# Kernel optimization log

Hardware: AMD Instinct MI355X
Metric: run time of the kernel (lower is better)

## Reference

```python
import jax, jax.numpy as jnp
import numpy as np

N = 30000      # nodes
E = 480000     # edges (no self loops; GATConv adds them)
IN = 256       # in_features
OUT = 128      # out_features == per-head channels (concat=False)
H = 4          # heads
NEG_SLOPE = 0.2


def setup_inputs() -> dict:
    key = jax.random.key(0)
    k = jax.random.split(key, 6)
    x = jax.random.normal(k[0], (N, IN), dtype=jnp.float32)
    src = jax.random.randint(k[1], (E,), 0, N, dtype=jnp.int32)
    # guarantee no self loops (GATConv would strip them before re-adding)
    off = jax.random.randint(k[2], (E,), 1, N, dtype=jnp.int32)
    dst = (src + off) % N
    edge_index = jnp.stack([src, dst])  # [2, E]
    W = jax.random.normal(k[3], (IN, H * OUT), dtype=jnp.float32) / np.float32(np.sqrt(IN))
    att_src = jax.random.normal(k[4], (H, OUT), dtype=jnp.float32) / np.float32(np.sqrt(OUT))
    att_dst = jax.random.normal(k[5], (H, OUT), dtype=jnp.float32) / np.float32(np.sqrt(OUT))
    bias = jnp.zeros((OUT,), dtype=jnp.float32)
    return {"x": x, "edge_index": edge_index, "W": W,
            "att_src": att_src, "att_dst": att_dst, "bias": bias}


def reference(x, edge_index, W, att_src, att_dst, bias):
    n = x.shape[0]
    # dense projection -> per-head features [N, H, C]
    h = (x @ W).reshape(n, H, OUT)
    a_s = jnp.einsum('nhc,hc->nh', h, att_src)  # [N, H]
    a_d = jnp.einsum('nhc,hc->nh', h, att_dst)  # [N, H]
    # add self loops (GATConv default add_self_loops=True)
    loop = jnp.arange(n, dtype=edge_index.dtype)
    src = jnp.concatenate([edge_index[0], loop])  # [Et]
    dst = jnp.concatenate([edge_index[1], loop])  # [Et]
    # per-edge attention logits + LeakyReLU
    alpha = jax.nn.leaky_relu(a_s[src] + a_d[dst], NEG_SLOPE)  # [Et, H]
    # segment softmax over incoming edges of each dst node
    amax = jax.ops.segment_max(alpha, dst, num_segments=n)      # [N, H]
    ex = jnp.exp(alpha - amax[dst])
    denom = jax.ops.segment_sum(ex, dst, num_segments=n)        # [N, H]
    w = ex / denom[dst]                                          # [Et, H]
    # gather source features, weight, scatter-add to dst
    msg = h[src] * w[:, :, None]                                 # [Et, H, C]
    out = jax.ops.segment_sum(msg, dst, num_segments=n)          # [N, H, C]
    # concat=False -> mean over heads, then bias, then module's tanh
    out = out.mean(axis=1) + bias                                # [N, C]
    return jnp.tanh(out)
```

## Files before the change

kernel.cpp:

```cpp
#include <hip/hip_runtime.h>
#include <math.h>

#define IN_F   256
#define OUT_F  128
#define HEADS  4
#define HD     (HEADS * OUT_F)
#define K2     1024
#define NEG    0.2f
#define CAP    64

typedef __attribute__((ext_vector_type(8))) short short8;
typedef __attribute__((ext_vector_type(4))) float f32x4;
typedef __attribute__((ext_vector_type(2))) float f32x2;

typedef __attribute__((address_space(1))) const void* gp_t;
typedef __attribute__((address_space(3))) void* lp_t;

static __device__ __forceinline__ ushort f2bf(float f) {
    union { float f; unsigned u; } v; v.f = f;
    unsigned r = (v.u + 0x7FFFu + ((v.u >> 16) & 1u)) >> 16;
    return (ushort)r;
}
static __device__ __forceinline__ float bflo(unsigned u) {
    union { unsigned u; float f; } v; v.u = u << 16; return v.f;
}
static __device__ __forceinline__ float bfhi(unsigned u) {
    union { unsigned u; float f; } v; v.u = u & 0xFFFF0000u; return v.f;
}

#define PKFMA(D, A, B) asm("v_pk_fma_f32 %0, %1, %2, %0" : "+v"(D) : "v"(A), "v"(B))

__global__ __launch_bounds__(256) void prep1(const float* __restrict__ W,
                                             const float* __restrict__ att_src,
                                             const float* __restrict__ att_dst,
                                             ushort* __restrict__ WT2,
                                             float* __restrict__ va_s,
                                             float* __restrict__ va_d,
                                             int* __restrict__ cursor,
                                             int n_nodes) {
    const int b = blockIdx.x;
    const int tid = threadIdx.x;
    if (b < 512) {
        int idx = b * 256 + tid;
        int cout = idx >> 10, kk = idx & 1023;
        int h = kk >> 8, c = kk & 255;
        WT2[idx] = f2bf(W[(size_t)c * HD + h * OUT_F + cout]);
    } else if (b < 768) {
        const int lane = tid & 63;
        const int p = (b - 512) * 4 + (tid >> 6);
        const int h = p >> 8;
        const int k = p & 255;
        const float* wr = W + (size_t)k * HD + h * OUT_F;
        float w0 = wr[lane], w1 = wr[lane + 64];
        float s0 = att_src[h * OUT_F + lane], s1 = att_src[h * OUT_F + lane + 64];
        float d0 = att_dst[h * OUT_F + lane], d1 = att_dst[h * OUT_F + lane + 64];
        float ss = w0 * s0 + w1 * s1;
        float sd = w0 * d0 + w1 * d1;
#pragma unroll
        for (int off = 32; off > 0; off >>= 1) {
            ss += __shfl_xor(ss, off, 64);
            sd += __shfl_xor(sd, off, 64);
        }
        if (lane == 0) { va_s[p] = ss; va_d[p] = sd; }
    } else {
        int i = (b - 768) * 256 + tid;
        if (i < n_nodes) cursor[i] = 0;
    }
}

__global__ __launch_bounds__(256) void prep2(const float* __restrict__ X,
                                             const float* __restrict__ va_s,
                                             const float* __restrict__ va_d,
                                             const int* __restrict__ src,
                                             const int* __restrict__ dst,
                                             ushort* __restrict__ Xb,
                                             float* __restrict__ a_s,
                                             float* __restrict__ a_d,
                                             int* __restrict__ cursor,
                                             int* __restrict__ table,
                                             int n_nodes, int n_edges, int nebk) {
    const int b = blockIdx.x;
    const int tid = threadIdx.x;
    if (b < nebk) {
        int e = b * 256 + tid;
        if (e < n_edges) {
            int d = dst[e];
            int r = atomicAdd(&cursor[d], 1);
            if (r < CAP) table[(size_t)d * CAP + r] = src[e];
        }
        return;
    }
    const int lane = tid & 63;
    const int node = (b - nebk) * 4 + (tid >> 6);
    if (node >= n_nodes) return;
    float4 v = *(const float4*)(X + (size_t)node * IN_F + lane * 4);
    ushort4 o; o.x = f2bf(v.x); o.y = f2bf(v.y); o.z = f2bf(v.z); o.w = f2bf(v.w);
    *(ushort4*)(Xb + (size_t)node * IN_F + lane * 4) = o;

    float ps[HEADS], pd[HEADS];
#pragma unroll
    for (int hd = 0; hd < HEADS; ++hd) {
        float4 s4 = *(const float4*)(va_s + hd * IN_F + lane * 4);
        float4 d4 = *(const float4*)(va_d + hd * IN_F + lane * 4);
        ps[hd] = v.x * s4.x + v.y * s4.y + v.z * s4.z + v.w * s4.w;
        pd[hd] = v.x * d4.x + v.y * d4.y + v.z * d4.z + v.w * d4.w;
    }
#pragma unroll
    for (int off = 32; off > 0; off >>= 1) {
#pragma unroll
        for (int hd = 0; hd < HEADS; ++hd) {
            ps[hd] += __shfl_xor(ps[hd], off, 64);
            pd[hd] += __shfl_xor(pd[hd], off, 64);
        }
    }
    if (lane == 0) {
        float4 s4 = make_float4(ps[0], ps[1], ps[2], ps[3]);
        float4 d4 = make_float4(pd[0], pd[1], pd[2], pd[3]);
        *(float4*)(a_s + node * 4) = s4;
        *(float4*)(a_d + node * 4) = d4;
    }
}

#define EDGE(E8)                                                            \
    {                                                                       \
        uint2 uu = *(const uint2*)(cons + (E8) * 512);                      \
        float4 wA = *(const float4*)(wp + (E8) * 8);                        \
        float4 wB = *(const float4*)(wp + (E8) * 8 + 4);                    \
        f32x2 f01 = {bflo(uu.x), bfhi(uu.x)};                               \
        f32x2 f23 = {bflo(uu.y), bfhi(uu.y)};                               \
        f32x2 w0p = {wA.x, wA.y}, w1p = {wA.z, wA.w};                       \
        f32x2 w2p = {wB.x, wB.y}, w3p = {wB.z, wB.w};                       \
        PKFMA(a01[0], f01, w0p); PKFMA(a23[0], f23, w0p);                   \
        PKFMA(a01[1], f01, w1p); PKFMA(a23[1], f23, w1p);                   \
        PKFMA(a01[2], f01, w2p); PKFMA(a23[2], f23, w2p);                   \
        PKFMA(a01[3], f01, w3p); PKFMA(a23[3], f23, w3p);                   \
    }

#define ISSUE(EB, DST)                                                      \
    {                                                                       \
        asm volatile("s_waitcnt lgkmcnt(0)" ::: "memory");                  \
        int s0_ = __shfl(sreg, (EB) + 0, 64);                               \
        int s1_ = __shfl(sreg, (EB) + 1, 64);                               \
        int s2_ = __shfl(sreg, (EB) + 2, 64);                               \
        int s3_ = __shfl(sreg, (EB) + 3, 64);                               \
        int s4_ = __shfl(sreg, (EB) + 4, 64);                               \
        int s5_ = __shfl(sreg, (EB) + 5, 64);                               \
        int s6_ = __shfl(sreg, (EB) + 6, 64);                               \
        int s7_ = __shfl(sreg, (EB) + 7, 64);                               \
        int sa_ = (lane & 32) ? s1_ : s0_;                                  \
        int sb_ = (lane & 32) ? s3_ : s2_;                                  \
        int sc_ = (lane & 32) ? s5_ : s4_;                                  \
        int sd_ = (lane & 32) ? s7_ : s6_;                                  \
        __builtin_amdgcn_global_load_lds((gp_t)(xb16 + (size_t)sa_ * 256),  \
                                         (lp_t)((DST) + 0 * 1024), 16, 0, 0);\
        __builtin_amdgcn_global_load_lds((gp_t)(xb16 + (size_t)sb_ * 256),  \
                                         (lp_t)((DST) + 1 * 1024), 16, 0, 0);\
        __builtin_amdgcn_global_load_lds((gp_t)(xb16 + (size_t)sc_ * 256),  \
                                         (lp_t)((DST) + 2 * 1024), 16, 0, 0);\
        __builtin_amdgcn_global_load_lds((gp_t)(xb16 + (size_t)sd_ * 256),  \
                                         (lp_t)((DST) + 3 * 1024), 16, 0, 0);\
    }

__global__ __launch_bounds__(256) void gat_agg(const ushort* __restrict__ Xb,
                                               const float* __restrict__ a_s,
                                               const float* __restrict__ a_d,
                                               const int* __restrict__ cursor,
                                               const int* __restrict__ table,
                                               ushort* __restrict__ Zb,
                                               int n_nodes) {
    __shared__ ushort xst[4][2][8][256];
    __shared__ float wse[4][CAP][8];
    const int lane = threadIdx.x & 63;
    const int wid  = threadIdx.x >> 6;
    const int n = blockIdx.x * 4 + wid;
    if (n >= n_nodes) return;
    int deg = cursor[n]; if (deg > CAP) deg = CAP;
    const int* row = table + (size_t)n * CAP;
    const bool act = lane < deg;
    int sreg = act ? row[lane] : n;

    const ushort* xb16 = Xb + (lane & 31) * 8;
    const uint2* xb2 = (const uint2*)Xb;
    uint2 uself = xb2[(size_t)n * 64 + lane];

    char* xb0 = (char*)&xst[wid][0][0][0];
    char* xb1 = (char*)&xst[wid][1][0][0];

    const int ntiles = (deg + 7) >> 3;
    if (ntiles > 0) ISSUE(0, xb0);

    const float4 ad4 = *(const float4*)(a_d + n * 4);
    const float4 as4 = *(const float4*)(a_s + n * 4);
    const float ad[4] = {ad4.x, ad4.y, ad4.z, ad4.w};
    float aself[4];
    {
        const float asn[4] = {as4.x, as4.y, as4.z, as4.w};
#pragma unroll
        for (int hd = 0; hd < 4; ++hd) {
            float al0 = asn[hd] + ad[hd];
            aself[hd] = al0 > 0.f ? al0 : NEG * al0;
        }
    }
    float al[4];
    {
        float4 av = *(const float4*)(a_s + (size_t)sreg * 4);
        const float as_[4] = {av.x, av.y, av.z, av.w};
#pragma unroll
        for (int hd = 0; hd < 4; ++hd) {
            float a = as_[hd] + ad[hd];
            a = a > 0.f ? a : NEG * a;
            al[hd] = act ? a : -1e30f;
        }
    }
    float m[4];
#pragma unroll
    for (int hd = 0; hd < 4; ++hd) m[hd] = al[hd];
#pragma unroll
    for (int off = 32; off > 0; off >>= 1)
#pragma unroll
        for (int hd = 0; hd < 4; ++hd)
            m[hd] = fmaxf(m[hd], __shfl_xor(m[hd], off, 64));
#pragma unroll
    for (int hd = 0; hd < 4; ++hd) m[hd] = fmaxf(m[hd], aself[hd]);

    float w[4], den[4];
#pragma unroll
    for (int hd = 0; hd < 4; ++hd) {
        w[hd] = act ? __expf(al[hd] - m[hd]) : 0.f;
        den[hd] = w[hd];
    }
#pragma unroll
    for (int off = 32; off > 0; off >>= 1)
#pragma unroll
        for (int hd = 0; hd < 4; ++hd)
            den[hd] += __shfl_xor(den[hd], off, 64);

    float es[4], rdv[4];
#pragma unroll
    for (int hd = 0; hd < 4; ++hd) {
        es[hd] = __expf(aself[hd] - m[hd]);
        rdv[hd] = 1.f / (den[hd] + es[hd]);
    }

    *(float4*)&wse[wid][lane][0] = make_float4(w[0], w[0], w[1], w[1]);
    *(float4*)&wse[wid][lane][4] = make_float4(w[2], w[2], w[3], w[3]);

    f32x2 a01[4], a23[4];
    {
        f32x2 s01 = {bflo(uself.x), bfhi(uself.x)};
        f32x2 s23 = {bflo(uself.y), bfhi(uself.y)};
#pragma unroll
        for (int hd = 0; hd < 4; ++hd) {
            f32x2 eh = {es[hd], es[hd]};
            a01[hd] = s01 * eh;
            a23[hd] = s23 * eh;
        }
    }
#pragma unroll 1
    for (int t = 0; t < ntiles; ++t) {
        if (t + 1 < ntiles) {
            ISSUE((t + 1) * 8, ((t + 1) & 1) ? xb1 : xb0);
            asm volatile("s_waitcnt vmcnt(4)" ::: "memory");
        } else {
            asm volatile("s_waitcnt vmcnt(0)" ::: "memory");
        }
        const char* cons = ((t & 1) ? xb1 : xb0) + lane * 8;
        const float* wp = &wse[wid][t * 8][0];
        EDGE(0); EDGE(1); EDGE(2); EDGE(3);
        EDGE(4); EDGE(5); EDGE(6); EDGE(7);
    }

    ushort* zr = Zb + (size_t)n * K2;
#pragma unroll
    for (int hd = 0; hd < 4; ++hd) {
        f32x2 r2 = {rdv[hd], rdv[hd]};
        f32x2 z01 = a01[hd] * r2;
        f32x2 z23 = a23[hd] * r2;
        ushort4 z;
        z.x = f2bf(z01.x); z.y = f2bf(z01.y);
        z.z = f2bf(z23.x); z.w = f2bf(z23.y);
        *(ushort4*)(zr + hd * 256 + lane * 4) = z;
    }
}

#define GBM 32
#define GBN 128
#define GBK 64

__global__ __launch_bounds__(256) void gemm2(const ushort* __restrict__ Zb,
                                             const ushort* __restrict__ WT2,
                                             const float* __restrict__ bias,
                                             float* __restrict__ out,
                                             int n_nodes) {
    __shared__ ushort As[2][GBM][GBK];
    __shared__ ushort Bs[2][GBN][GBK];
    const int tid = threadIdx.x;
    const int m0 = blockIdx.y * GBM;
    const int wave = tid >> 6, lane = tid & 63;
    const int wm = (wave & 1) * 16, wn = (wave >> 1) * 64;
    const int l15 = lane & 15, quad = lane >> 4;

    const int rr8 = lane >> 3;
    const int cg  = (lane & 7) ^ rr8;
    const ushort* gA0 = Zb + (size_t)(m0 + wave * 8 + rr8) * K2 + cg * 8;
    const ushort* gB0 = WT2 + (size_t)(wave * 32 + rr8) * K2 + cg * 8;
    const ushort* gB1 = gB0 + 8 * K2;
    const ushort* gB2 = gB0 + 16 * K2;
    const ushort* gB3 = gB0 + 24 * K2;

#define STAGE(T, B)                                                          \
    {                                                                        \
        const int ko_ = (T) * GBK;                                           \
        __builtin_amdgcn_global_load_lds((gp_t)(gA0 + ko_),                  \
            (lp_t)&As[B][wave * 8][0], 16, 0, 0);                            \
        __builtin_amdgcn_global_load_lds((gp_t)(gB0 + ko_),                  \
            (lp_t)&Bs[B][wave * 32][0], 16, 0, 0);                           \
        __builtin_amdgcn_global_load_lds((gp_t)(gB1 + ko_),                  \
            (lp_t)&Bs[B][wave * 32 + 8][0], 16, 0, 0);                       \
        __builtin_amdgcn_global_load_lds((gp_t)(gB2 + ko_),                  \
            (lp_t)&Bs[B][wave * 32 + 16][0], 16, 0, 0);                      \
        __builtin_amdgcn_global_load_lds((gp_t)(gB3 + ko_),                  \
            (lp_t)&Bs[B][wave * 32 + 24][0], 16, 0, 0);                      \
    }

    f32x4 acc[4];
#pragma unroll
    for (int j = 0; j < 4; ++j) acc[j] = (f32x4){0.f, 0.f, 0.f, 0.f};

    const int NT = K2 / GBK;
    STAGE(0, 0);
#pragma unroll 1
    for (int t = 0; t < NT; ++t) {
        const int b = t & 1;
        if (t + 1 < NT) {
            STAGE(t + 1, b ^ 1);
            asm volatile("s_waitcnt vmcnt(5)" ::: "memory");
        } else {
            asm volatile("s_waitcnt vmcnt(0)" ::: "memory");
        }
        asm volatile("s_barrier" ::: "memory");

#pragma unroll
        for (int tt = 0; tt < 2; ++tt) {
            const int sl = ((tt * 4 + quad) ^ (l15 & 7)) * 8;
            short8 af = *(const short8*)&As[b][wm + l15][sl];
            short8 bf_[4];
#pragma unroll
            for (int fn = 0; fn < 4; ++fn)
                bf_[fn] = *(const short8*)&Bs[b][wn + fn * 16 + l15][sl];
#pragma unroll
            for (int fn = 0; fn < 4; ++fn)
                acc[fn] = __builtin_amdgcn_mfma_f32_16x16x32_bf16(
                    af, bf_[fn], acc[fn], 0, 0, 0);
        }
        asm volatile("s_barrier" ::: "memory");
    }

    float bcol[4];
#pragma unroll
    for (int fn = 0; fn < 4; ++fn) bcol[fn] = bias[wn + fn * 16 + l15];

    int gmb = m0 + wm + quad * 4;
#pragma unroll
    for (int reg = 0; reg < 4; ++reg) {
        int gm = gmb + reg;
        if (gm < n_nodes) {
#pragma unroll
            for (int fn = 0; fn < 4; ++fn) {
                float o = tanhf(0.25f * acc[fn][reg] + bcol[fn]);
                out[(size_t)gm * OUT_F + wn + fn * 16 + l15] = o;
            }
        }
    }
}

extern "C" void kernel_launch(void* const* d_in, const int* in_sizes, int n_in,
                              void* d_out, int out_size, void* d_ws, size_t ws_size,
                              hipStream_t stream) {
    const float* x       = (const float*)d_in[0];
    const int*   ei      = (const int*)d_in[1];
    const float* W       = (const float*)d_in[2];
    const float* att_src = (const float*)d_in[3];
    const float* att_dst = (const float*)d_in[4];
    const float* bias    = (const float*)d_in[5];
    float* out = (float*)d_out;

    const int n_nodes = in_sizes[0] / IN_F;
    const int n_edges = in_sizes[1] / 2;
    const int* src = ei;
    const int* dst = ei + n_edges;

    char* ws = (char*)d_ws;
    size_t off = 0;
    auto alloc = [&](size_t bytes) -> void* {
        void* p = ws + off;
        off = (off + bytes + 255) & ~(size_t)255;
        return p;
    };
    ushort* Xb     = (ushort*)alloc((size_t)n_nodes * IN_F * sizeof(ushort));
    ushort* Zb     = (ushort*)alloc((size_t)n_nodes * K2 * sizeof(ushort));
    ushort* WT2    = (ushort*)alloc((size_t)OUT_F * K2 * sizeof(ushort));
    float*  va_s   = (float*)alloc((size_t)HEADS * IN_F * sizeof(float));
    float*  va_d   = (float*)alloc((size_t)HEADS * IN_F * sizeof(float));
    float*  a_s    = (float*)alloc((size_t)n_nodes * HEADS * sizeof(float));
    float*  a_d    = (float*)alloc((size_t)n_nodes * HEADS * sizeof(float));
    int*    cursor = (int*)alloc((size_t)n_nodes * sizeof(int));
    int*    table  = (int*)alloc((size_t)n_nodes * CAP * sizeof(int));
    (void)ws_size; (void)n_in; (void)out_size;

    const int czb  = (n_nodes + 255) / 256;
    const int nebk = (n_edges + 255) / 256;

    prep1<<<768 + czb, 256, 0, stream>>>(W, att_src, att_dst, WT2, va_s, va_d,
                                         cursor, n_nodes);
    prep2<<<nebk + (n_nodes + 3) / 4, 256, 0, stream>>>(x, va_s, va_d, src, dst,
                                                        Xb, a_s, a_d, cursor, table,
                                                        n_nodes, n_edges, nebk);
    gat_agg<<<(n_nodes + 3) / 4, 256, 0, stream>>>(Xb, a_s, a_d, cursor, table,
                                                   Zb, n_nodes);

    dim3 ggrid(1, (n_nodes + GBM - 1) / GBM);
    gemm2<<<ggrid, 256, 0, stream>>>(Zb, WT2, bias, out, n_nodes);
}
```

Before: 197.0 us.

## Partition edge bucketing by destination range across blocks with vectorized edge loads

The edge-bucketing phase of prep2 now splits destinations into 8 contiguous node ranges. Each group of 8 blocks reads the same 1024-edge chunk, and each block only handles edges whose destination falls in its range. Edge indices are loaded as int4 vectors. The aim is better L2 locality for the cursor atomics and the table writes, since the 8 blocks in a group likely run together on the same XCD. The cost is that every edge is read 8 times and there are 8x as many bucketing blocks.

```diff
diff --git a/kernel.cpp b/kernel.cpp
--- a/kernel.cpp
+++ b/kernel.cpp
@@ -68,6 +68,12 @@
     }
 }
 
+#define PROC(DD, SS)                                                        \
+    if ((unsigned)((DD) - lo) < (unsigned)nr) {                             \
+        int r_ = atomicAdd(&cursor[DD], 1);                                 \
+        if (r_ < CAP) table[(size_t)(DD) * CAP + r_] = (SS);                \
+    }
+
 __global__ __launch_bounds__(256) void prep2(const float* __restrict__ X,
                                              const float* __restrict__ va_s,
                                              const float* __restrict__ va_d,
@@ -78,20 +84,30 @@
                                              float* __restrict__ a_d,
                                              int* __restrict__ cursor,
                                              int* __restrict__ table,
-                                             int n_nodes, int n_edges, int nebk) {
+                                             int n_nodes, int n_edges,
+                                             int ntb, int nr) {
     const int b = blockIdx.x;
     const int tid = threadIdx.x;
-    if (b < nebk) {
-        int e = b * 256 + tid;
-        if (e < n_edges) {
-            int d = dst[e];
-            int r = atomicAdd(&cursor[d], 1);
-            if (r < CAP) table[(size_t)d * CAP + r] = src[e];
+    if (b < ntb) {
+        const int g = b & 7;
+        const int chunk = b >> 3;
+        const int e0 = chunk * 1024 + tid * 4;
+        const int lo = g * nr;
+        if (e0 + 4 <= n_edges) {
+            int4 s4 = *(const int4*)(src + e0);
+            int4 d4 = *(const int4*)(dst + e0);
+            PROC(d4.x, s4.x); PROC(d4.y, s4.y);
+            PROC(d4.z, s4.z); PROC(d4.w, s4.w);
+        } else if (e0 < n_edges) {
+            for (int i = 0; e0 + i < n_edges; ++i) {
+                int dd = dst[e0 + i], ss = src[e0 + i];
+                PROC(dd, ss);
+            }
         }
         return;
     }
     const int lane = tid & 63;
-    const int node = (b - nebk) * 4 + (tid >> 6);
+    const int node = (b - ntb) * 4 + (tid >> 6);
     if (node >= n_nodes) return;
     float4 v = *(const float4*)(X + (size_t)node * IN_F + lane * 4);
     ushort4 o; o.x = f2bf(v.x); o.y = f2bf(v.y); o.z = f2bf(v.z); o.w = f2bf(v.w);
@@ -409,13 +425,15 @@
     (void)ws_size; (void)n_in; (void)out_size;
 
     const int czb  = (n_nodes + 255) / 256;
-    const int nebk = (n_edges + 255) / 256;
+    const int nech = (n_edges + 1023) / 1024;
+    const int ntb  = nech * 8;
+    const int nr   = (n_nodes + 7) / 8;
 
     prep1<<<768 + czb, 256, 0, stream>>>(W, att_src, att_dst, WT2, va_s, va_d,
                                          cursor, n_nodes);
-    prep2<<<nebk + (n_nodes + 3) / 4, 256, 0, stream>>>(x, va_s, va_d, src, dst,
-                                                        Xb, a_s, a_d, cursor, table,
-                                                        n_nodes, n_edges, nebk);
+    prep2<<<ntb + (n_nodes + 3) / 4, 256, 0, stream>>>(x, va_s, va_d, src, dst,
+                                                       Xb, a_s, a_d, cursor, table,
+                                                       n_nodes, n_edges, ntb, nr);
     gat_agg<<<(n_nodes + 3) / 4, 256, 0, stream>>>(Xb, a_s, a_d, cursor, table,
                                                    Zb, n_nodes);
 
```

Result: no change. 194.7 us (-1.2%).
